# Kernel optimization log

Hardware: AMD Instinct MI355X
Metric: run time of the kernel (lower is better)

## Reference

```python
import jax, jax.numpy as jnp
import numpy as np

D = 128       # embed_dim
UD = 128      # user_embed_dim
NU, NI, NR = 100000, 50000, 10
B, H, S = 4096, 50, 32
EPS = 1e-5


def setup_inputs() -> dict:
    key = jax.random.key(0)
    ks = jax.random.split(key, 24)
    p = lambda k, s: (jax.random.normal(k, s, jnp.float32) * 0.05)
    inp = {
        'u2e': p(ks[0], (NU, D)), 'v2e': p(ks[1], (NI, D)), 'r2e': p(ks[2], (NR, D)),
        'gv_w1': p(ks[3], (2 * D, D)), 'gv_b1': jnp.zeros(D),
        'gv_w2': p(ks[4], (D, D)), 'gv_b2': jnp.zeros(D),
        'atth_w1': p(ks[5], (2 * D, D)), 'atth_b1': jnp.zeros(D),
        'atth_w2': p(ks[6], (D, 1)), 'atth_b2': jnp.zeros(1),
        'enc_w': p(ks[7], (2 * D, D)), 'enc_b': jnp.zeros(D),
        'atts_w1': p(ks[8], (2 * D, D)), 'atts_b1': jnp.zeros(D),
        'atts_w2': p(ks[9], (D, 1)), 'atts_b2': jnp.zeros(1),
        'soc_w': p(ks[10], (2 * D, D)), 'soc_b': jnp.zeros(D),
        'attn_wa': p(ks[11], (D, D)), 'attn_ba': p(ks[12], (D,)),
        'fc1_w': p(ks[13], (D, D)), 'fc1_b': jnp.zeros(D),
        'bn1_g': jnp.ones(D), 'bn1_b': jnp.zeros(D),
        'fc2_w': p(ks[14], (D, UD)), 'fc2_b': jnp.zeros(UD),
        'efc1_w': p(ks[15], (2 * UD, D)), 'efc1_b': jnp.zeros(D),
        'bn2_g': jnp.ones(D), 'bn2_b': jnp.zeros(D),
        'efc2_w': p(ks[16], (D, UD)), 'efc2_b': jnp.zeros(UD),
        'user_ids': jax.random.randint(ks[17], (B, 2), 0, NU),
        'hist_items': jax.random.randint(ks[18], (2 * B, H), 0, NI),
        'hist_ratings': jax.random.randint(ks[19], (2 * B, H), 0, NR),
        'soc_neigh': jax.random.randint(ks[20], (2 * B, S), 0, NU),
    }
    return inp


def _forward(u2e, v2e, r2e, gv_w1, gv_b1, gv_w2, gv_b2, atth_w1, atth_b1, atth_w2, atth_b2,
             enc_w, enc_b, atts_w1, atts_b1, atts_w2, atts_b2, soc_w, soc_b, attn_wa, attn_ba,
             fc1_w, fc1_b, bn1_g, bn1_b, fc2_w, fc2_b, efc1_w, efc1_b, bn2_g, bn2_b,
             efc2_w, efc2_b, user_ids, hist_items, hist_ratings, soc_neigh):
    u = u2e[user_ids.reshape(-1)]                                   # [N,D]
    # --- UV_Aggregator: rating-history aggregation with attention ---
    x = jnp.concatenate([v2e[hist_items], r2e[hist_ratings]], -1)   # [N,H,2D]
    x = jax.nn.relu(x @ gv_w1 + gv_b1)
    x = jax.nn.relu(x @ gv_w2 + gv_b2)                              # [N,H,D]
    q = jnp.broadcast_to(u[:, None, :], x.shape)
    e = jax.nn.relu(jnp.concatenate([x, q], -1) @ atth_w1 + atth_b1) @ atth_w2 + atth_b2
    a = jax.nn.softmax(e, axis=1)                                   # [N,H,1]
    agg = jnp.sum(a * x, axis=1)                                    # [N,D]
    # --- UV_Encoder ---
    h_hist = jax.nn.relu(jnp.concatenate([u, agg], -1) @ enc_w + enc_b)
    # --- Social_Aggregator: neighbor aggregation with attention ---
    nf = u2e[soc_neigh]                                             # [N,S,D]
    qn = jnp.broadcast_to(u[:, None, :], nf.shape)
    es = jax.nn.relu(jnp.concatenate([nf, qn], -1) @ atts_w1 + atts_b1) @ atts_w2 + atts_b2
    a_s = jax.nn.softmax(es, axis=1)
    agg_s = jnp.sum(a_s * nf, axis=1)                               # [N,D]
    # --- Social_Encoder ---
    h = jax.nn.relu(jnp.concatenate([h_hist, agg_s], -1) @ soc_w + soc_b)
    hp = h.reshape(-1, 2, D)                                        # [B,2,D] (initiator, respondent)
    # --- SelfAttentionBatch over each pair ---
    ap = jax.nn.softmax(jnp.tanh(hp @ attn_wa) @ attn_ba, axis=1)   # [B,2]
    w = ap[..., None] * hp                                          # [B,2,D]
    # --- social project head: fc1 -> BN (per-pair batch of 2, train mode) -> relu -> fc2 ---
    y = w @ fc1_w + fc1_b                                           # [B,2,D]
    mu = y.mean(axis=1, keepdims=True)
    var = y.var(axis=1, keepdims=True)
    y = (y - mu) * jax.lax.rsqrt(var + EPS) * bn1_g + bn1_b
    y = jax.nn.relu(y) @ fc2_w + fc2_b                              # [B,2,UD]
    ini, res = y[:, 0], y[:, 1]
    # --- esocial head on concatenated pair reps: fc -> BN over batch -> relu -> fc ---
    c = y.reshape(y.shape[0], -1)                                   # [B,2*UD]
    z = c @ efc1_w + efc1_b                                         # [B,D]
    z = (z - z.mean(0)) * jax.lax.rsqrt(z.var(0) + EPS) * bn2_g + bn2_b
    z = jax.nn.relu(z) @ efc2_w + efc2_b                            # [B,UD]
    return z, ini, res


def reference(u2e, v2e, r2e, gv_w1, gv_b1, gv_w2, gv_b2, atth_w1, atth_b1, atth_w2, atth_b2,
              enc_w, enc_b, atts_w1, atts_b1, atts_w2, atts_b2, soc_w, soc_b, attn_wa, attn_ba,
              fc1_w, fc1_b, bn1_g, bn1_b, fc2_w, fc2_b, efc1_w, efc1_b, bn2_g, bn2_b,
              efc2_w, efc2_b, user_ids, hist_items, hist_ratings, soc_neigh):
    return _forward(u2e, v2e, r2e, gv_w1, gv_b1, gv_w2, gv_b2, atth_w1, atth_b1, atth_w2,
                    atth_b2, enc_w, enc_b, atts_w1, atts_b1, atts_w2, atts_b2, soc_w, soc_b,
                    attn_wa, attn_ba, fc1_w, fc1_b, bn1_g, bn1_b, fc2_w, fc2_b, efc1_w,
                    efc1_b, bn2_g, bn2_b, efc2_w, efc2_b, user_ids, hist_items,
                    hist_ratings, soc_neigh)
```

## Files before the change

### kernel.cpp

```cpp
#include <hip/hip_runtime.h>
#include <hip/hip_bf16.h>
#include <math.h>

#define NROWS   8192
#define HLEN    50
#define SLEN    32
#define NPAIR   4096

typedef __attribute__((ext_vector_type(8))) short   short8;
typedef __attribute__((ext_vector_type(8))) __bf16  b8;
typedef __attribute__((ext_vector_type(4))) float   f32x4;
typedef unsigned short us;

#define A_GV_B1    0
#define A_GV_B2    128
#define A_ATTH_B1  256
#define A_ATTH_W2  384
#define A_ENC_W    512
#define A_ENC_B    33280
#define A_ATTS_B1  33408
#define A_ATTS_W2  33536
#define A_SOC_W    33664
#define A_SOC_B    66432
#define A_ATTN_WA  66560
#define A_ATTN_BA  82944
#define A_FC1_W    83072
#define A_FC1_B    99456
#define A_BN1_G    99584
#define A_BN1_B    99712
#define A_FC2_W    99840
#define A_FC2_B    116224
#define A_EFC1_W   116352
#define A_EFC1_B   149120
#define A_BN2_G    149248
#define A_BN2_B    149376
#define A_EFC2_W   149504
#define A_EFC2_B   165888
#define A_TOTAL    166016

#define WS_HR    0u
#define WS_Z     2097152u
#define WS_ST    4194304u
#define WS_WP1   4195328u
#define WS_WP2   4260864u
#define WS_WPA   4293632u
#define WS_WPS   4359168u
#define WS_AR    4424704u
#define WS_UB    4757504u
#define WS_VB    30357504u
#define WS_RB    43157504u
#define WS2_NEED 43160064u

#define PB_CVT   649
#define PB_PACK  56
#define PB_TAB   9376

__device__ __forceinline__ float b2f(us u){
  unsigned int x = ((unsigned int)u) << 16; float f;
  __builtin_memcpy(&f, &x, 4); return f;
}
__device__ __forceinline__ us f2b(float f){
  unsigned int x; __builtin_memcpy(&x, &f, 4);
  return (us)((x + 0x7fffu + ((x >> 16) & 1u)) >> 16);
}
__device__ __forceinline__ us f2bc(float f){
  unsigned int x; __builtin_memcpy(&x, &f, 4);
  return (us)((x + 0x8000u) >> 16);
}
__device__ __forceinline__ float relu(float x){ return 0.5f * (x + fabsf(x)); }

__device__ __forceinline__ b8 f8_to_b8(const float* f){
  short8 v;
#pragma unroll
  for (int j = 0; j < 8; ++j) v[j] = (short)f2bc(f[j]);
  return __builtin_bit_cast(b8, v);
}

typedef __attribute__((address_space(3))) unsigned char lds_b;
typedef const __attribute__((address_space(1))) unsigned char glob_b;

__device__ __forceinline__ void gll16(const us* g, us* d){
  __builtin_amdgcn_global_load_lds((glob_b*)g, (lds_b*)d, 16, 0, 0);
}

__device__ __forceinline__ void stage8k(const us* __restrict__ W, us* sB,
                                        int w8, int l, int ks, int p){
  const us* src = W + ((long)ks << 12) + (w8 << 9) + (l << 3);
  us* dst = sB + (p << 12) + (w8 << 9);
  gll16(src, dst);
}

struct Prep {
  const void* cp[24]; unsigned coff[25];
  const float *W1, *W2, *WA, *WS;
  const float *u2e, *v2e, *r2e;
};
__global__ void k_prep(Prep pr, us* __restrict__ AR,
                       us* __restrict__ Wp1, us* __restrict__ Wp2,
                       us* __restrict__ WpA, us* __restrict__ WpS,
                       us* __restrict__ Ub, us* __restrict__ Vb,
                       us* __restrict__ Rb, int do_tab)
{
  const int b = blockIdx.x, t = threadIdx.x;
  if (b < PB_CVT){
    int i = b * 256 + t;
    if (i >= A_TOTAL) return;
    int s = 0;
    while (i >= (int)pr.coff[s + 1]) ++s;
    AR[i] = f2b(((const float*)pr.cp[s])[i - (int)pr.coff[s]]);
  } else if (b < PB_CVT + PB_PACK){
    int g = (b - PB_CVT) * 256 + t;
    const float* W; us* Wp; int loc;
    if      (g <  4096){ W = pr.W1; Wp = Wp1; loc = g; }
    else if (g <  6144){ W = pr.W2; Wp = Wp2; loc = g - 4096; }
    else if (g < 10240){ W = pr.WA; Wp = WpA; loc = g - 6144; }
    else               { W = pr.WS; Wp = WpS; loc = g - 10240; }
    int lane16 = loc & 15, quad = (loc >> 4) & 3, nt = (loc >> 6) & 7, kseg = loc >> 9;
#pragma unroll
    for (int j = 0; j < 8; ++j)
      Wp[(long)loc * 8 + j] = f2b(W[(kseg * 32 + quad * 8 + j) * 128 + nt * 16 + lane16]);
  } else {
    if (!do_tab) return;
    int i = (b - PB_CVT - PB_PACK) * 256 + t;
    const float* s; us* d; int loc;
    if      (i < 1600000){ s = pr.u2e; d = Ub; loc = i; }
    else if (i < 2400000){ s = pr.v2e; d = Vb; loc = i - 1600000; }
    else if (i < 2400160){ s = pr.r2e; d = Rb; loc = i - 2400000; }
    else return;
    const float* sp = s + (long)loc * 8;
    short8 w;
#pragma unroll
    for (int j = 0; j < 8; ++j) w[j] = (short)f2b(sp[j]);
    *(short8*)(d + (long)loc * 8) = w;
  }
}

template<int TAB>
__global__ __launch_bounds__(512, 4)
void k_fused(const int* __restrict__ items, const int* __restrict__ ratings,
             const void* __restrict__ vt, const void* __restrict__ rt,
             const int* __restrict__ uids, const void* __restrict__ ut,
             const int* __restrict__ soc,
             const us* __restrict__ Wp1, const us* __restrict__ Wp2,
             const us* __restrict__ WpA, const us* __restrict__ WpS,
             const us* __restrict__ AR, us* __restrict__ HR)
{
  const int t = threadIdx.x;
  const int rr = t >> 8, tt = t & 255;
  const int r = blockIdx.x * 2 + rr;
  const int w = tt >> 6;
  const int w8 = t >> 6;
  const int l = t & 63, lane16 = l & 15, quad = l >> 4;
  const int tc = tt & 127, th = tt >> 7;
  const long ubase = (long)uids[r] * 128;

  __shared__ __align__(16) us sX[2][64 * 136];
  __shared__ __align__(16) us sB[2 * 4096];
  __shared__ float esh[2][64], a_sh[2][64], part[2][256], xin[2][256];

  stage8k(Wp1, sB, w8, l, 0, 0);

  const int arow = w * 16 + lane16;
  const bool av = arow < HLEN;
  const int it_i = av ? items[r * HLEN + arow]   : 0;
  const int rt_i = av ? ratings[r * HLEN + arow] : 0;

  b8 af[8];
#pragma unroll
  for (int ks = 0; ks < 8; ++ks){
    b8 a;
    if constexpr (TAB){
      const us* ap = (ks < 4)
          ? (const us*)vt + (long)it_i * 128 + ks * 32 + quad * 8
          : (const us*)rt + (long)rt_i * 128 + (ks - 4) * 32 + quad * 8;
      a = *(const b8*)ap;
    } else {
      const float* ap = (ks < 4)
          ? (const float*)vt + (long)it_i * 128 + ks * 32 + quad * 8
          : (const float*)rt + (long)rt_i * 128 + (ks - 4) * 32 + quad * 8;
      a = f8_to_b8(ap);
    }
    if (!av) a = __builtin_bit_cast(b8, (short8)0);
    af[ks] = a;
  }
  b8 uf[4];
#pragma unroll
  for (int ks = 0; ks < 4; ++ks){
    if constexpr (TAB)
      uf[ks] = *(const b8*)((const us*)ut + ubase + ks * 32 + quad * 8);
    else
      uf[ks] = f8_to_b8((const float*)ut + ubase + ks * 32 + quad * 8);
  }

  {
    f32x4 acc[8];
#pragma unroll
    for (int nt = 0; nt < 8; ++nt) acc[nt] = (f32x4){0.f,0.f,0.f,0.f};
#pragma unroll
    for (int ks = 0; ks < 8; ++ks){
      __syncthreads();
      if (ks < 7) stage8k(Wp1, sB, w8, l, ks + 1, (ks + 1) & 1);
      else        stage8k(Wp2, sB, w8, l, 0, 0);
      const us* bb = sB + ((ks & 1) << 12) + l * 8;
#pragma unroll
      for (int nt = 0; nt < 8; ++nt)
        acc[nt] = __builtin_amdgcn_mfma_f32_16x16x32_bf16(
            af[ks], *(const b8*)(bb + nt * 512), acc[nt], 0, 0, 0);
    }
#pragma unroll
    for (int nt = 0; nt < 8; ++nt){
      int col = nt * 16 + lane16;
      float bbv = b2f(AR[A_GV_B1 + col]);
#pragma unroll
      for (int rg = 0; rg < 4; ++rg)
        sX[rr][(w * 16 + quad * 4 + rg) * 136 + col] = f2bc(relu(acc[nt][rg] + bbv));
    }
  }

  {
    b8 a2[4];
#pragma unroll
    for (int ks = 0; ks < 4; ++ks)
      a2[ks] = *(const b8*)(sX[rr] + arow * 136 + ks * 32 + quad * 8);
    f32x4 acc[8];
#pragma unroll
    for (int nt = 0; nt < 8; ++nt) acc[nt] = (f32x4){0.f,0.f,0.f,0.f};
#pragma unroll
    for (int ks = 0; ks < 4; ++ks){
      __syncthreads();
      if (ks < 3) stage8k(Wp2, sB, w8, l, ks + 1, (ks + 1) & 1);
      else        stage8k(WpA, sB, w8, l, 0, 0);
      const us* bb = sB + ((ks & 1) << 12) + l * 8;
#pragma unroll
      for (int nt = 0; nt < 8; ++nt)
        acc[nt] = __builtin_amdgcn_mfma_f32_16x16x32_bf16(
            a2[ks], *(const b8*)(bb + nt * 512), acc[nt], 0, 0, 0);
    }
#pragma unroll
    for (int nt = 0; nt < 8; ++nt){
      int col = nt * 16 + lane16;
      float bbv = b2f(AR[A_GV_B2 + col]);
#pragma unroll
      for (int rg = 0; rg < 4; ++rg)
        sX[rr][(w * 16 + quad * 4 + rg) * 136 + col] = f2bc(relu(acc[nt][rg] + bbv));
    }
  }

  {
    b8 a3[8];
#pragma unroll
    for (int ks = 0; ks < 4; ++ks)
      a3[ks] = *(const b8*)(sX[rr] + arow * 136 + ks * 32 + quad * 8);
#pragma unroll
    for (int ks = 0; ks < 4; ++ks) a3[4 + ks] = uf[ks];
    f32x4 acc[8];
#pragma unroll
    for (int nt = 0; nt < 8; ++nt) acc[nt] = (f32x4){0.f,0.f,0.f,0.f};
#pragma unroll
    for (int ks = 0; ks < 8; ++ks){
      __syncthreads();
      if (ks < 7) stage8k(WpA, sB, w8, l, ks + 1, (ks + 1) & 1);
      else        stage8k(WpS, sB, w8, l, 0, 0);
      const us* bb = sB + ((ks & 1) << 12) + l * 8;
#pragma unroll
      for (int nt = 0; nt < 8; ++nt)
        acc[nt] = __builtin_amdgcn_mfma_f32_16x16x32_bf16(
            a3[ks], *(const b8*)(bb + nt * 512), acc[nt], 0, 0, 0);
    }
    float pr[4] = {0.f, 0.f, 0.f, 0.f};
#pragma unroll
    for (int nt = 0; nt < 8; ++nt){
      int col = nt * 16 + lane16;
      float bbv = b2f(AR[A_ATTH_B1 + col]);
      float wwv = b2f(AR[A_ATTH_W2 + col]);
#pragma unroll
      for (int rg = 0; rg < 4; ++rg)
        pr[rg] += relu(acc[nt][rg] + bbv) * wwv;
    }
#pragma unroll
    for (int rg = 0; rg < 4; ++rg){
      float p = pr[rg];
      p += __shfl_xor(p, 1, 64);
      p += __shfl_xor(p, 2, 64);
      p += __shfl_xor(p, 4, 64);
      p += __shfl_xor(p, 8, 64);
      if (lane16 == 0) esh[rr][w * 16 + quad * 4 + rg] = p;
    }
  }
  __syncthreads();

  if (tt < 64){
    float e = (tt < HLEN) ? esh[rr][tt] : -1e30f;
    float mx = e;
#pragma unroll
    for (int m = 1; m < 64; m <<= 1) mx = fmaxf(mx, __shfl_xor(mx, m, 64));
    float ex = (tt < HLEN) ? expf(e - mx) : 0.f;
    float s = ex;
#pragma unroll
    for (int m = 1; m < 64; m <<= 1) s += __shfl_xor(s, m, 64);
    if (tt < HLEN) a_sh[rr][tt] = ex / s;
  }
  __syncthreads();

  {
    float s = 0.f;
    for (int h = th * 25; h < th * 25 + 25; ++h)
      s += a_sh[rr][h] * b2f(sX[rr][h * 136 + tc]);
    part[rr][tt] = s;
  }
  __syncthreads();
  if (tt < 128){
    xin[rr][tt] = TAB ? b2f(((const us*)ut)[ubase + tt]) : ((const float*)ut)[ubase + tt];
    xin[rr][128 + tt] = part[rr][tt] + part[rr][128 + tt];
  }
  __syncthreads();

  {
    float s0 = 0.f, s1 = 0.f;
    const int kb = th * 128;
    for (int k = 0; k < 128; k += 2){
      s0 += xin[rr][kb + k]     * b2f(AR[A_ENC_W + (kb + k)     * 128 + tc]);
      s1 += xin[rr][kb + k + 1] * b2f(AR[A_ENC_W + (kb + k + 1) * 128 + tc]);
    }
    part[rr][tt] = s0 + s1;
#pragma unroll
    for (int it = 0; it < 2; ++it){
      int idx = tt * 8 + it * 2048;
      int row = idx >> 7, col = idx & 127;
      long eb = (long)soc[r * SLEN + row] * 128 + col;
      short8 v;
      if constexpr (TAB) v = *(const short8*)((const us*)ut + eb);
      else               v = __builtin_bit_cast(short8, f8_to_b8((const float*)ut + eb));
      *(short8*)(sX[rr] + row * 136 + col) = v;
    }
  }
  __syncthreads();

  float hhv = 0.f;
  if (tt < 128)
    hhv = relu(part[rr][tt] + part[rr][128 + tt] + b2f(AR[A_ENC_B + tt]));

  {
    const int mt = w & 1, nh = w >> 1;
    const int arow2 = mt * 16 + lane16;
    b8 aS[8];
#pragma unroll
    for (int ks = 0; ks < 4; ++ks)
      aS[ks] = *(const b8*)(sX[rr] + arow2 * 136 + ks * 32 + quad * 8);
#pragma unroll
    for (int ks = 0; ks < 4; ++ks) aS[4 + ks] = uf[ks];
    f32x4 acc[4];
#pragma unroll
    for (int nt = 0; nt < 4; ++nt) acc[nt] = (f32x4){0.f,0.f,0.f,0.f};
#pragma unroll
    for (int ks = 0; ks < 8; ++ks){
      __syncthreads();
      if (ks < 7) stage8k(WpS, sB, w8, l, ks + 1, (ks + 1) & 1);
      const us* bb = sB + ((ks & 1) << 12) + (nh << 11) + l * 8;
#pragma unroll
      for (int nt = 0; nt < 4; ++nt)
        acc[nt] = __builtin_amdgcn_mfma_f32_16x16x32_bf16(
            aS[ks], *(const b8*)(bb + nt * 512), acc[nt], 0, 0, 0);
    }
    float pr[4] = {0.f, 0.f, 0.f, 0.f};
#pragma unroll
    for (int nt = 0; nt < 4; ++nt){
      int n = nh * 64 + nt * 16 + lane16;
      float bbv = b2f(AR[A_ATTS_B1 + n]);
      float wwv = b2f(AR[A_ATTS_W2 + n]);
#pragma unroll
      for (int rg = 0; rg < 4; ++rg)
        pr[rg] += relu(acc[nt][rg] + bbv) * wwv;
    }
#pragma unroll
    for (int rg = 0; rg < 4; ++rg){
      float p = pr[rg];
      p += __shfl_xor(p, 1, 64);
      p += __shfl_xor(p, 2, 64);
      p += __shfl_xor(p, 4, 64);
      p += __shfl_xor(p, 8, 64);
      if (lane16 == 0) esh[rr][nh * 32 + mt * 16 + quad * 4 + rg] = p;
    }
  }
  __syncthreads();

  if (tt < 32){
    float e = esh[rr][tt] + esh[rr][32 + tt];
    float mx = e;
#pragma unroll
    for (int m = 1; m < 32; m <<= 1) mx = fmaxf(mx, __shfl_xor(mx, m, 32));
    float ex = expf(e - mx);
    float s = ex;
#pragma unroll
    for (int m = 1; m < 32; m <<= 1) s += __shfl_xor(s, m, 32);
    a_sh[rr][tt] = ex / s;
  }
  __syncthreads();

  {
    float s = 0.f;
    for (int h = th * 16; h < th * 16 + 16; ++h)
      s += a_sh[rr][h] * b2f(sX[rr][h * 136 + tc]);
    part[rr][tt] = s;
  }
  __syncthreads();
  if (tt < 128){
    xin[rr][tt]       = hhv;
    xin[rr][128 + tt] = part[rr][tt] + part[rr][128 + tt];
  }
  __syncthreads();

  {
    float s0 = 0.f, s1 = 0.f;
    const int kb = th * 128;
    for (int k = 0; k < 128; k += 2){
      s0 += xin[rr][kb + k]     * b2f(AR[A_SOC_W + (kb + k)     * 128 + tc]);
      s1 += xin[rr][kb + k + 1] * b2f(AR[A_SOC_W + (kb + k + 1) * 128 + tc]);
    }
    part[rr][tt] = s0 + s1;
  }
  __syncthreads();
  if (tt < 128)
    HR[(long)r * 128 + tt] =
        f2bc(relu(part[rr][tt] + part[rr][128 + tt] + b2f(AR[A_SOC_B + tt])));
}

__global__ void k7_head(const us* __restrict__ HR, const us* __restrict__ AR,
                        float* __restrict__ OUT, float* __restrict__ Z)
{
  const int i = blockIdx.x, t = threadIdx.x;
  __shared__ float hp[2][128], ry[2][128], csh[256];
  __shared__ float sred[2][2];

  hp[0][t] = b2f(HR[(long)(2 * i)     * 128 + t]);
  hp[1][t] = b2f(HR[(long)(2 * i + 1) * 128 + t]);
  __syncthreads();

  float a0 = 0.f, a1 = 0.f, b0 = 0.f, b1 = 0.f;
  for (int k = 0; k < 128; k += 2){
    float w0 = b2f(AR[A_ATTN_WA + k * 128 + t]);
    float w1 = b2f(AR[A_ATTN_WA + (k + 1) * 128 + t]);
    a0 += hp[0][k] * w0;  a1 += hp[0][k + 1] * w1;
    b0 += hp[1][k] * w0;  b1 += hp[1][k + 1] * w1;
  }
  float ba = b2f(AR[A_ATTN_BA + t]);
  float p0 = tanhf(a0 + a1) * ba;
  float p1 = tanhf(b0 + b1) * ba;
#pragma unroll
  for (int m = 1; m < 64; m <<= 1){ p0 += __shfl_xor(p0, m, 64); p1 += __shfl_xor(p1, m, 64); }
  if ((t & 63) == 0){ sred[t >> 6][0] = p0; sred[t >> 6][1] = p1; }
  __syncthreads();

  float s0 = sred[0][0] + sred[1][0], s1 = sred[0][1] + sred[1][1];
  float mx = fmaxf(s0, s1);
  float e0 = expf(s0 - mx), e1 = expf(s1 - mx);
  float aj0 = e0 / (e0 + e1), aj1 = e1 / (e0 + e1);

  a0 = 0.f; a1 = 0.f; b0 = 0.f; b1 = 0.f;
  for (int k = 0; k < 128; k += 2){
    float w0 = b2f(AR[A_FC1_W + k * 128 + t]);
    float w1 = b2f(AR[A_FC1_W + (k + 1) * 128 + t]);
    a0 += hp[0][k] * w0;  a1 += hp[0][k + 1] * w1;
    b0 += hp[1][k] * w0;  b1 += hp[1][k + 1] * w1;
  }
  float fb = b2f(AR[A_FC1_B + t]);
  float y0 = aj0 * (a0 + a1) + fb;
  float y1 = aj1 * (b0 + b1) + fb;

  {
    float mu = 0.5f * (y0 + y1);
    float dv = 0.5f * (y0 - y1);
    float rs = rsqrtf(dv * dv + 1e-5f);
    float g = b2f(AR[A_BN1_G + t]), bb = b2f(AR[A_BN1_B + t]);
    ry[0][t] = relu((y0 - mu) * rs * g + bb);
    ry[1][t] = relu((y1 - mu) * rs * g + bb);
  }
  __syncthreads();

  a0 = 0.f; a1 = 0.f; b0 = 0.f; b1 = 0.f;
  for (int k = 0; k < 128; k += 2){
    float w0 = b2f(AR[A_FC2_W + k * 128 + t]);
    float w1 = b2f(AR[A_FC2_W + (k + 1) * 128 + t]);
    a0 += ry[0][k] * w0;  a1 += ry[0][k + 1] * w1;
    b0 += ry[1][k] * w0;  b1 += ry[1][k + 1] * w1;
  }
  float cb = b2f(AR[A_FC2_B + t]);
  float y2_0 = a0 + a1 + cb;
  float y2_1 = b0 + b1 + cb;
  OUT[(long)NPAIR * 128     + (long)i * 128 + t] = y2_0;
  OUT[(long)2 * NPAIR * 128 + (long)i * 128 + t] = y2_1;
  csh[t]       = y2_0;
  csh[128 + t] = y2_1;
  __syncthreads();

  {
    float v0 = 0.f, v1 = 0.f;
    for (int k = 0; k < 128; k += 2){
      v0 += csh[k]     * b2f(AR[A_EFC1_W + k * 128 + t]);
      v1 += csh[k + 1] * b2f(AR[A_EFC1_W + (k + 1) * 128 + t]);
    }
    float p20 = v0 + v1;
    v0 = 0.f; v1 = 0.f;
    for (int k = 0; k < 128; k += 2){
      v0 += csh[128 + k]     * b2f(AR[A_EFC1_W + (128 + k) * 128 + t]);
      v1 += csh[128 + k + 1] * b2f(AR[A_EFC1_W + (128 + k + 1) * 128 + t]);
    }
    float p21 = v0 + v1;
    Z[(long)i * 128 + t] = p20 + p21 + b2f(AR[A_EFC1_B + t]);
  }
}

__global__ void k8_stats(const float* __restrict__ Z, float* __restrict__ ST){
  const int c = blockIdx.x, t = threadIdx.x;
  float s = 0.f, s2 = 0.f;
  for (int row = t; row < NPAIR; row += 256){
    float v = Z[(long)row * 128 + c];
    s += v; s2 += v * v;
  }
#pragma unroll
  for (int m = 1; m < 64; m <<= 1){ s += __shfl_xor(s, m, 64); s2 += __shfl_xor(s2, m, 64); }
  __shared__ float red[8];
  if ((t & 63) == 0){ red[t >> 6] = s; red[4 + (t >> 6)] = s2; }
  __syncthreads();
  if (t == 0){
    float S  = red[0] + red[1] + red[2] + red[3];
    float S2 = red[4] + red[5] + red[6] + red[7];
    float mean = S / (float)NPAIR;
    float var  = S2 / (float)NPAIR - mean * mean;
    ST[c]       = mean;
    ST[128 + c] = rsqrtf(var + 1e-5f);
  }
}

__global__ void k9_final(const float* __restrict__ Z, const float* __restrict__ ST,
                         const us* __restrict__ AR, float* __restrict__ OUT)
{
  const int t = threadIdx.x;
  const int d = t & 127, h = t >> 7;
  const long r0 = (long)blockIdx.x * 8;
  __shared__ float zn[8][132];

  float stm = ST[d], str = ST[128 + d];
  float g = b2f(AR[A_BN2_G + d]), bb = b2f(AR[A_BN2_B + d]);
#pragma unroll
  for (int q = 0; q < 4; ++q){
    int row = h * 4 + q;
    float zv = Z[(r0 + row) * 128 + d];
    zn[row][d] = relu((zv - stm) * str * g + bb);
  }
  __syncthreads();

  float a0[4] = {0.f,0.f,0.f,0.f}, a1[4] = {0.f,0.f,0.f,0.f};
  for (int k = 0; k < 128; k += 2){
    float w0 = b2f(AR[A_EFC2_W + k * 128 + d]);
    float w1 = b2f(AR[A_EFC2_W + (k + 1) * 128 + d]);
#pragma unroll
    for (int q = 0; q < 4; ++q){
      a0[q] += zn[h * 4 + q][k]     * w0;
      a1[q] += zn[h * 4 + q][k + 1] * w1;
    }
  }
  float eb = b2f(AR[A_EFC2_B + d]);
#pragma unroll
  for (int q = 0; q < 4; ++q)
    OUT[(r0 + h * 4 + q) * 128 + d] = a0[q] + a1[q] + eb;
}

extern "C" void kernel_launch(void* const* d_in, const int* in_sizes, int n_in,
                              void* d_out, int out_size, void* d_ws, size_t ws_size,
                              hipStream_t stream)
{
  const float* u2e = (const float*)d_in[0];
  const float* v2e = (const float*)d_in[1];
  const float* r2e = (const float*)d_in[2];
  const int* user_ids     = (const int*)d_in[33];
  const int* hist_items   = (const int*)d_in[34];
  const int* hist_ratings = (const int*)d_in[35];
  const int* soc_neigh    = (const int*)d_in[36];

  char* ws = (char*)d_ws;
  us*    HR  = (us*)(ws + WS_HR);
  float* Z   = (float*)(ws + WS_Z);
  float* ST  = (float*)(ws + WS_ST);
  us*    Wp1 = (us*)(ws + WS_WP1);
  us*    Wp2 = (us*)(ws + WS_WP2);
  us*    WpA = (us*)(ws + WS_WPA);
  us*    WpS = (us*)(ws + WS_WPS);
  us*    AR  = (us*)(ws + WS_AR);
  us*    Ub  = (us*)(ws + WS_UB);
  us*    Vb  = (us*)(ws + WS_VB);
  us*    Rb  = (us*)(ws + WS_RB);
  float* OUT = (float*)d_out;

  const bool big = ws_size >= (size_t)WS2_NEED;

  Prep pr;
  const void* sp[24] = {d_in[4], d_in[6], d_in[8], d_in[9], d_in[11], d_in[12],
                        d_in[14], d_in[15], d_in[17], d_in[18], d_in[19], d_in[20],
                        d_in[21], d_in[22], d_in[23], d_in[24], d_in[25], d_in[26],
                        d_in[27], d_in[28], d_in[29], d_in[30], d_in[31], d_in[32]};
  const unsigned offs[25] = {0,128,256,384,512,33280,33408,33536,33664,66432,
                             66560,82944,83072,99456,99584,99712,99840,116224,
                             116352,149120,149248,149376,149504,165888,166016};
  for (int i = 0; i < 24; ++i) pr.cp[i] = sp[i];
  for (int i = 0; i < 25; ++i) pr.coff[i] = offs[i];
  pr.W1 = (const float*)d_in[3];  pr.W2 = (const float*)d_in[5];
  pr.WA = (const float*)d_in[7];  pr.WS = (const float*)d_in[13];
  pr.u2e = u2e; pr.v2e = v2e; pr.r2e = r2e;

  const int prep_blocks = big ? (PB_CVT + PB_PACK + PB_TAB) : (PB_CVT + PB_PACK);
  k_prep<<<prep_blocks, 256, 0, stream>>>(pr, AR, Wp1, Wp2, WpA, WpS,
                                          Ub, Vb, Rb, big ? 1 : 0);

  if (big){
    k_fused<1><<<NROWS / 2, 512, 0, stream>>>(hist_items, hist_ratings, Vb, Rb,
        user_ids, Ub, soc_neigh, Wp1, Wp2, WpA, WpS, AR, HR);
  } else {
    k_fused<0><<<NROWS / 2, 512, 0, stream>>>(hist_items, hist_ratings, v2e, r2e,
        user_ids, u2e, soc_neigh, Wp1, Wp2, WpA, WpS, AR, HR);
  }

  k7_head<<<NPAIR, 128, 0, stream>>>(HR, AR, OUT, Z);
  k8_stats<<<128, 256, 0, stream>>>(Z, ST);
  k9_final<<<NPAIR / 8, 256, 0, stream>>>(Z, ST, AR, OUT);
}
```

Before: 467.3 us.

## Triple-buffer weight staging with partial vmcnt waits instead of full syncthreads

Result: no change. 464.4 us (median of 3 runs) (-0.6%).

```diff
diff --git a/kernel.cpp b/kernel.cpp
--- a/kernel.cpp
+++ b/kernel.cpp
@@ -86,9 +86,16 @@
 __device__ __forceinline__ void stage8k(const us* __restrict__ W, us* sB,
                                         int w8, int l, int ks, int p){
   const us* src = W + ((long)ks << 12) + (w8 << 9) + (l << 3);
-  us* dst = sB + (p << 12) + (w8 << 9);
+  us* dst = sB + p * 4096 + (w8 << 9);
   gll16(src, dst);
 }
+
+#define PHASE_SYNC() do {                                   \
+    asm volatile("s_waitcnt vmcnt(1)" ::: "memory");        \
+    __builtin_amdgcn_s_barrier();                           \
+    asm volatile("" ::: "memory");                          \
+    __builtin_amdgcn_sched_barrier(0);                      \
+  } while (0)
 
 struct Prep {
   const void* cp[24]; unsigned coff[25];
@@ -155,10 +162,11 @@
   const long ubase = (long)uids[r] * 128;
 
   __shared__ __align__(16) us sX[2][64 * 136];
-  __shared__ __align__(16) us sB[2 * 4096];
+  __shared__ __align__(16) us sB[3 * 4096];
   __shared__ float esh[2][64], a_sh[2][64], part[2][256], xin[2][256];
 
   stage8k(Wp1, sB, w8, l, 0, 0);
+  stage8k(Wp1, sB, w8, l, 1, 1);
 
   const int arow = w * 16 + lane16;
   const bool av = arow < HLEN;
@@ -198,10 +206,11 @@
     for (int nt = 0; nt < 8; ++nt) acc[nt] = (f32x4){0.f,0.f,0.f,0.f};
 #pragma unroll
     for (int ks = 0; ks < 8; ++ks){
-      __syncthreads();
-      if (ks < 7) stage8k(Wp1, sB, w8, l, ks + 1, (ks + 1) & 1);
-      else        stage8k(Wp2, sB, w8, l, 0, 0);
-      const us* bb = sB + ((ks & 1) << 12) + l * 8;
+      PHASE_SYNC();
+      if      (ks < 6)  stage8k(Wp1, sB, w8, l, ks + 2, (ks + 2) % 3);
+      else if (ks == 6) stage8k(Wp2, sB, w8, l, 0, 2);
+      else              stage8k(Wp2, sB, w8, l, 1, 0);
+      const us* bb = sB + (ks % 3) * 4096 + l * 8;
 #pragma unroll
       for (int nt = 0; nt < 8; ++nt)
         acc[nt] = __builtin_amdgcn_mfma_f32_16x16x32_bf16(
@@ -227,10 +236,11 @@
     for (int nt = 0; nt < 8; ++nt) acc[nt] = (f32x4){0.f,0.f,0.f,0.f};
 #pragma unroll
     for (int ks = 0; ks < 4; ++ks){
-      __syncthreads();
-      if (ks < 3) stage8k(Wp2, sB, w8, l, ks + 1, (ks + 1) & 1);
-      else        stage8k(WpA, sB, w8, l, 0, 0);
-      const us* bb = sB + ((ks & 1) << 12) + l * 8;
+      PHASE_SYNC();
+      if      (ks < 2)  stage8k(Wp2, sB, w8, l, ks + 2, (ks + 10) % 3);
+      else if (ks == 2) stage8k(WpA, sB, w8, l, 0, 0);
+      else              stage8k(WpA, sB, w8, l, 1, 1);
+      const us* bb = sB + ((8 + ks) % 3) * 4096 + l * 8;
 #pragma unroll
       for (int nt = 0; nt < 8; ++nt)
         acc[nt] = __builtin_amdgcn_mfma_f32_16x16x32_bf16(
@@ -258,10 +268,11 @@
     for (int nt = 0; nt < 8; ++nt) acc[nt] = (f32x4){0.f,0.f,0.f,0.f};
 #pragma unroll
     for (int ks = 0; ks < 8; ++ks){
-      __syncthreads();
-      if (ks < 7) stage8k(WpA, sB, w8, l, ks + 1, (ks + 1) & 1);
-      else        stage8k(WpS, sB, w8, l, 0, 0);
-      const us* bb = sB + ((ks & 1) << 12) + l * 8;
+      PHASE_SYNC();
+      if      (ks < 6)  stage8k(WpA, sB, w8, l, ks + 2, (ks + 14) % 3);
+      else if (ks == 6) stage8k(WpS, sB, w8, l, 0, 2);
+      else              stage8k(WpS, sB, w8, l, 1, 0);
+      const us* bb = sB + ((12 + ks) % 3) * 4096 + l * 8;
 #pragma unroll
       for (int nt = 0; nt < 8; ++nt)
         acc[nt] = __builtin_amdgcn_mfma_f32_16x16x32_bf16(
@@ -354,9 +365,9 @@
     for (int nt = 0; nt < 4; ++nt) acc[nt] = (f32x4){0.f,0.f,0.f,0.f};
 #pragma unroll
     for (int ks = 0; ks < 8; ++ks){
-      __syncthreads();
-      if (ks < 7) stage8k(WpS, sB, w8, l, ks + 1, (ks + 1) & 1);
-      const us* bb = sB + ((ks & 1) << 12) + (nh << 11) + l * 8;
+      PHASE_SYNC();
+      if (ks < 6) stage8k(WpS, sB, w8, l, ks + 2, (ks + 22) % 3);
+      const us* bb = sB + ((20 + ks) % 3) * 4096 + (nh << 11) + l * 8;
 #pragma unroll
       for (int nt = 0; nt < 4; ++nt)
         acc[nt] = __builtin_amdgcn_mfma_f32_16x16x32_bf16(
```
